# Optimization experiments

Hardware: AMD Instinct MI355X
Metric: run time of the kernel (lower is better)

## Reference

```python
import jax, jax.numpy as jnp
import numpy as np

MAX_DEPTH = 12  # 2^12-1 = 4095 internal nodes, 4096 leaves
NUM_INPUT = 1024
NUM_OUTPUT = 1024
BATCH = 4096


def setup_inputs() -> dict:
    key = jax.random.key(0)
    k1, k2, k3 = jax.random.split(key, 3)
    n_internal = (1 << MAX_DEPTH) - 1
    n_leaves = 1 << MAX_DEPTH
    x = jax.random.normal(k1, (BATCH, NUM_INPUT), dtype=jnp.float32)
    # per-node weights ~ N(0, 0.1) as in nn.Parameter(torch.empty(num_input).normal_(0, 0.1))
    W = jax.random.normal(k2, (n_internal, NUM_INPUT), dtype=jnp.float32) * 0.1
    b = jnp.zeros((n_internal,), dtype=jnp.float32)
    # leaf prob_dist initialized to ones in the original
    leaf = jnp.ones((n_leaves, NUM_OUTPUT), dtype=jnp.float32)
    # use random leaves so the blend is non-trivial for correctness checking
    leaf = leaf + jax.random.normal(k3, (n_leaves, NUM_OUTPUT), dtype=jnp.float32)
    return {"x": x, "W": W, "b": b, "leaf": leaf}


def reference(x, W, b, leaf):
    # W rows are internal nodes in level order: [root | level1 (2) | level2 (4) | ...]
    # Gate value at each node: sigmoid(x . w + b); output blends right with weight g,
    # left with weight (1-g), recursively -> leaf mixture weights are products of
    # gate / (1-gate) along each root-to-leaf path.
    B = x.shape[0]
    g = jax.nn.sigmoid(jnp.einsum('bi,ni->bn', x, W) + b)  # [B, n_internal]
    probs = jnp.ones((B, 1), dtype=x.dtype)
    idx = 0
    for d in range(MAX_DEPTH):  # structural loop over tree levels (fixed, small)
        n = 1 << d
        gl = g[:, idx:idx + n]  # gates at level d, [B, n]
        idx += n
        # children interleaved: [L0, R0, L1, R1, ...]; left weight (1-g), right g
        probs = jnp.stack([probs * (1.0 - gl), probs * gl], axis=-1).reshape(B, 2 * n)
    # output = sum over leaves of path_prob * leaf_dist
    out = jnp.einsum('bl,lo->bo', probs, leaf)  # [B, num_output]
    return out
```

## Files before the change

kernel.cpp:

```cpp
#include <hip/hip_runtime.h>
#include <hip/hip_bf16.h>
#include <hip/hip_fp16.h>

typedef _Float16 half8 __attribute__((ext_vector_type(8)));
typedef _Float16 half4 __attribute__((ext_vector_type(4)));
typedef float floatx4 __attribute__((ext_vector_type(4)));

#define BATCH   4096
#define NIN     1024
#define NODES   4095
#define NPAD    4096
#define NOUT    1024
#define NLEAF   4096
#define SPLITK  4

__device__ __forceinline__ void gload_lds16(const void* g, void* l) {
    __builtin_amdgcn_global_load_lds(
        (const __attribute__((address_space(1))) void*)g,
        (__attribute__((address_space(3))) void*)l, 16, 0, 0);
}

__global__ void k_prep(const float* __restrict__ x, const float* __restrict__ W,
                       const float* __restrict__ leaf,
                       _Float16* __restrict__ xh, _Float16* __restrict__ Wh,
                       _Float16* __restrict__ leafT) {
    __shared__ _Float16 t[32][33];
    const int b = blockIdx.x;
    if (b < 4096) {
        int i = (b * 256 + threadIdx.x) * 4;
        float4 v = *(const float4*)(x + i);
        half4 h;
        h.x = (_Float16)v.x; h.y = (_Float16)v.y;
        h.z = (_Float16)v.z; h.w = (_Float16)v.w;
        *(half4*)(xh + i) = h;
    } else if (b < 8192) {
        int i = ((b - 4096) * 256 + threadIdx.x) * 4;
        float4 v;
        if (i < NODES * NIN) v = *(const float4*)(W + i);
        else                 v = make_float4(0.f, 0.f, 0.f, 0.f);
        half4 h;
        h.x = (_Float16)v.x; h.y = (_Float16)v.y;
        h.z = (_Float16)v.z; h.w = (_Float16)v.w;
        *(half4*)(Wh + i) = h;
    } else {
        int tb = b - 8192;
        int l0 = (tb & 127) * 32, o0 = (tb >> 7) * 32;
        int tx = threadIdx.x & 31, ty = threadIdx.x >> 5;
#pragma unroll
        for (int i = 0; i < 4; i++) {
            int l = l0 + ty + i * 8;
            t[ty + i * 8][tx] = (_Float16)leaf[(size_t)l * NOUT + o0 + tx];
        }
        __syncthreads();
#pragma unroll
        for (int i = 0; i < 4; i++) {
            int o = o0 + ty + i * 8;
            leafT[(size_t)o * NLEAF + l0 + tx] = t[tx][ty + i * 8];
        }
    }
}

template <int EPILOGUE>
__launch_bounds__(1024, 4)
__global__ void gemm256(const _Float16* __restrict__ A,
                        const _Float16* __restrict__ Bm,
                        const float* __restrict__ bias,
                        void* __restrict__ C,
                        int M, int N, int K, int ldc, int Klen) {
    __shared__ __align__(16) _Float16 As[2 * 16384];
    __shared__ __align__(16) _Float16 Bs[2 * 16384];
    const int tid  = threadIdx.x;
    const int lane = tid & 63;
    const int wid  = tid >> 6;
    const int wm   = wid >> 2;
    const int wn   = wid & 3;
    const int m0 = blockIdx.y * 256;
    const int n0 = blockIdx.x * 256;
    const int k0 = blockIdx.z * Klen;
    (void)N;

    floatx4 acc[4][4] = {};

    const int hh = tid >> 9;
    const int rr = (tid >> 2) & 127;
    const int cc = (tid & 3) ^ ((tid >> 3) & 3);
    const _Float16* Abase = A  + (size_t)(m0 + hh * 128 + rr) * K + k0 + cc * 8;
    const _Float16* Bbase = Bm + (size_t)(n0 + hh * 128 + rr) * K + k0 + cc * 8;
    const int dsl = hh * 8192 + (tid & 511) * 8;

    auto stage = [&](int bufx, int T) {
        const int d = bufx * 16384 + dsl;
        gload_lds16(Abase + T * 64,      &As[d]);
        gload_lds16(Abase + T * 64 + 32, &As[d + 4096]);
        gload_lds16(Bbase + T * 64,      &Bs[d]);
        gload_lds16(Bbase + T * 64 + 32, &Bs[d + 4096]);
    };

    const int l15 = lane & 15;
    const int l4  = lane >> 4;
    const int pos = (l4 ^ ((l15 >> 1) & 3)) * 8;
    const int aoff = ((wm & 1) * 64 + l15) * 32 + pos + (wm >> 1) * 8192;
    const int boff = ((wn & 1) * 64 + l15) * 32 + pos + (wn >> 1) * 8192;

    auto compute = [&](int bufx) {
#pragma unroll
        for (int s = 0; s < 2; s++) {
            const _Float16* Ab = &As[bufx * 16384 + s * 4096 + aoff];
            const _Float16* Bb = &Bs[bufx * 16384 + s * 4096 + boff];
            half8 af[4], bf[4];
#pragma unroll
            for (int fi = 0; fi < 4; fi++)
                af[fi] = *(const half8*)(Ab + fi * 512);
#pragma unroll
            for (int fj = 0; fj < 4; fj++)
                bf[fj] = *(const half8*)(Bb + fj * 512);
#pragma unroll
            for (int fi = 0; fi < 4; fi++)
#pragma unroll
                for (int fj = 0; fj < 4; fj++)
                    acc[fi][fj] = __builtin_amdgcn_mfma_f32_16x16x32_f16(
                        af[fi], bf[fj], acc[fi][fj], 0, 0, 0);
        }
    };

    const int NTt = Klen >> 6;

    stage(0, 0);
    __syncthreads();
    for (int T = 0; T < NTt; T += 2) {
        if (T + 1 < NTt) stage(1, T + 1);
        compute(0);
        __syncthreads();
        if (T + 2 < NTt) stage(0, T + 2);
        if (T + 1 < NTt) compute(1);
        __syncthreads();
    }

    _Float16* Cp = (_Float16*)C + (EPILOGUE == 2 ? (size_t)blockIdx.z * M * ldc : 0);
#pragma unroll
    for (int fi = 0; fi < 4; fi++)
#pragma unroll
        for (int fj = 0; fj < 4; fj++) {
            const int col = n0 + wn * 64 + fj * 16 + l15;
            float bb = 0.f;
            if (EPILOGUE == 1) bb = (col < NODES) ? bias[col] : 0.f;
#pragma unroll
            for (int rj = 0; rj < 4; rj++) {
                const int row = m0 + wm * 64 + fi * 16 + l4 * 4 + rj;
                float v = acc[fi][fj][rj];
                if (EPILOGUE == 1) {
                    float z = v + bb;
                    Cp[(size_t)row * ldc + col] = (_Float16)(1.f / (1.f + __expf(-z)));
                } else {
                    Cp[(size_t)row * ldc + col] = (_Float16)v;
                }
            }
        }
}

__global__ void k_reduce4(const _Float16* __restrict__ part, float* __restrict__ out) {
    const size_t S = (size_t)BATCH * NOUT;
    size_t i = ((size_t)blockIdx.x * 256 + threadIdx.x) * 8;
    half8 a = *(const half8*)(part + i);
    half8 b = *(const half8*)(part + S + i);
    half8 c = *(const half8*)(part + 2 * S + i);
    half8 d = *(const half8*)(part + 3 * S + i);
    float4 lo, hi;
    lo.x = (float)a[0] + (float)b[0] + (float)c[0] + (float)d[0];
    lo.y = (float)a[1] + (float)b[1] + (float)c[1] + (float)d[1];
    lo.z = (float)a[2] + (float)b[2] + (float)c[2] + (float)d[2];
    lo.w = (float)a[3] + (float)b[3] + (float)c[3] + (float)d[3];
    hi.x = (float)a[4] + (float)b[4] + (float)c[4] + (float)d[4];
    hi.y = (float)a[5] + (float)b[5] + (float)c[5] + (float)d[5];
    hi.z = (float)a[6] + (float)b[6] + (float)c[6] + (float)d[6];
    hi.w = (float)a[7] + (float)b[7] + (float)c[7] + (float)d[7];
    *(float4*)(out + i) = lo;
    *(float4*)(out + i + 4) = hi;
}

__global__ void k_probs(const _Float16* __restrict__ g,
                        _Float16* __restrict__ probs) {
    __shared__ float gs[NPAD];
    const int b = blockIdx.x;
    const _Float16* grow = g + (size_t)b * NPAD;
#pragma unroll
    for (int it = 0; it < 2; it++) {
        int i = threadIdx.x + it * 256;
        half8 v = *(const half8*)(grow + i * 8);
#pragma unroll
        for (int j = 0; j < 8; j++) gs[i * 8 + j] = (float)v[j];
    }
    __syncthreads();
    const int t = threadIdx.x;
    float p = 1.f;
#pragma unroll
    for (int d = 0; d < 8; d++) {
        int node = (1 << d) - 1 + (t >> (8 - d));
        float gg = gs[node];
        int bit = (t >> (7 - d)) & 1;
        p *= bit ? gg : (1.f - gg);
    }
    float p9[2], p10[4], p11[8], p12[16];
    {
        float gg = gs[255 + t];
        p9[0] = p * (1.f - gg); p9[1] = p * gg;
    }
#pragma unroll
    for (int i = 0; i < 2; i++) {
        float gg = gs[511 + 2 * t + i];
        p10[2 * i] = p9[i] * (1.f - gg); p10[2 * i + 1] = p9[i] * gg;
    }
#pragma unroll
    for (int i = 0; i < 4; i++) {
        float gg = gs[1023 + 4 * t + i];
        p11[2 * i] = p10[i] * (1.f - gg); p11[2 * i + 1] = p10[i] * gg;
    }
#pragma unroll
    for (int i = 0; i < 8; i++) {
        float gg = gs[2047 + 8 * t + i];
        p12[2 * i] = p11[i] * (1.f - gg); p12[2 * i + 1] = p11[i] * gg;
    }
    half8 o0, o1;
#pragma unroll
    for (int j = 0; j < 8; j++) { o0[j] = (_Float16)p12[j]; o1[j] = (_Float16)p12[8 + j]; }
    _Float16* pr = probs + (size_t)b * NLEAF + t * 16;
    *(half8*)(pr) = o0;
    *(half8*)(pr + 8) = o1;
}

extern "C" void kernel_launch(void* const* d_in, const int* in_sizes, int n_in,
                              void* d_out, int out_size, void* d_ws, size_t ws_size,
                              hipStream_t stream) {
    (void)in_sizes; (void)n_in; (void)out_size; (void)ws_size;
    const float* x    = (const float*)d_in[0];
    const float* W    = (const float*)d_in[1];
    const float* bias = (const float*)d_in[2];
    const float* leaf = (const float*)d_in[3];
    float* out = (float*)d_out;

    _Float16* base  = (_Float16*)d_ws;
    _Float16* leafT = base;
    _Float16* probs = base + (size_t)4 * 1024 * 1024;
    _Float16* xh    = base + (size_t)20 * 1024 * 1024;
    _Float16* Wh    = base + (size_t)24 * 1024 * 1024;
    _Float16* g     = base + (size_t)28 * 1024 * 1024;
    _Float16* part  = xh;

    k_prep<<<12288, 256, 0, stream>>>(x, W, leaf, xh, Wh, leafT);

    gemm256<1><<<dim3(NPAD / 256, BATCH / 256, 1), 1024, 0, stream>>>(
        xh, Wh, bias, (void*)g, BATCH, NPAD, NIN, NPAD, NIN);

    k_probs<<<BATCH, 256, 0, stream>>>(g, probs);

    gemm256<2><<<dim3(NOUT / 256, BATCH / 256, SPLITK), 1024, 0, stream>>>(
        probs, leafT, nullptr, (void*)part, BATCH, NOUT, NLEAF, NOUT, NLEAF / SPLITK);

    k_reduce4<<<(BATCH * NOUT) / (256 * 8), 256, 0, stream>>>(part, out);
}
```

Baseline: 109.9 us.

## Switch GEMM to triple-buffered 32-wide K tiles with one raw barrier per step

```diff
diff --git a/kernel.cpp b/kernel.cpp
--- a/kernel.cpp
+++ b/kernel.cpp
@@ -19,6 +19,8 @@
         (const __attribute__((address_space(1))) void*)g,
         (__attribute__((address_space(3))) void*)l, 16, 0, 0);
 }
+
+#define RBAR() asm volatile("s_barrier" ::: "memory")
 
 __global__ void k_prep(const float* __restrict__ x, const float* __restrict__ W,
                        const float* __restrict__ leaf,
@@ -67,8 +69,8 @@
                         const float* __restrict__ bias,
                         void* __restrict__ C,
                         int M, int N, int K, int ldc, int Klen) {
-    __shared__ __align__(16) _Float16 As[2 * 16384];
-    __shared__ __align__(16) _Float16 Bs[2 * 16384];
+    __shared__ __align__(16) _Float16 As[3 * 8192];
+    __shared__ __align__(16) _Float16 Bs[3 * 8192];
     const int tid  = threadIdx.x;
     const int lane = tid & 63;
     const int wid  = tid >> 6;
@@ -81,60 +83,63 @@
 
     floatx4 acc[4][4] = {};
 
-    const int hh = tid >> 9;
-    const int rr = (tid >> 2) & 127;
+    const int rr = tid >> 2;
     const int cc = (tid & 3) ^ ((tid >> 3) & 3);
-    const _Float16* Abase = A  + (size_t)(m0 + hh * 128 + rr) * K + k0 + cc * 8;
-    const _Float16* Bbase = Bm + (size_t)(n0 + hh * 128 + rr) * K + k0 + cc * 8;
-    const int dsl = hh * 8192 + (tid & 511) * 8;
+    const _Float16* Abase = A  + (size_t)(m0 + rr) * K + k0 + cc * 8;
+    const _Float16* Bbase = Bm + (size_t)(n0 + rr) * K + k0 + cc * 8;
+    const int dsl = tid * 8;
 
     auto stage = [&](int bufx, int T) {
-        const int d = bufx * 16384 + dsl;
-        gload_lds16(Abase + T * 64,      &As[d]);
-        gload_lds16(Abase + T * 64 + 32, &As[d + 4096]);
-        gload_lds16(Bbase + T * 64,      &Bs[d]);
-        gload_lds16(Bbase + T * 64 + 32, &Bs[d + 4096]);
+        gload_lds16(Abase + T * 32, &As[bufx * 8192 + dsl]);
+        gload_lds16(Bbase + T * 32, &Bs[bufx * 8192 + dsl]);
     };
 
     const int l15 = lane & 15;
     const int l4  = lane >> 4;
     const int pos = (l4 ^ ((l15 >> 1) & 3)) * 8;
-    const int aoff = ((wm & 1) * 64 + l15) * 32 + pos + (wm >> 1) * 8192;
-    const int boff = ((wn & 1) * 64 + l15) * 32 + pos + (wn >> 1) * 8192;
+    const int aoff = (wm * 64 + l15) * 32 + pos;
+    const int boff = (wn * 64 + l15) * 32 + pos;
 
     auto compute = [&](int bufx) {
-#pragma unroll
-        for (int s = 0; s < 2; s++) {
-            const _Float16* Ab = &As[bufx * 16384 + s * 4096 + aoff];
-            const _Float16* Bb = &Bs[bufx * 16384 + s * 4096 + boff];
-            half8 af[4], bf[4];
-#pragma unroll
-            for (int fi = 0; fi < 4; fi++)
-                af[fi] = *(const half8*)(Ab + fi * 512);
+        const _Float16* Ab = &As[bufx * 8192 + aoff];
+        const _Float16* Bb = &Bs[bufx * 8192 + boff];
+        half8 af[4], bf[4];
+#pragma unroll
+        for (int fi = 0; fi < 4; fi++)
+            af[fi] = *(const half8*)(Ab + fi * 512);
+#pragma unroll
+        for (int fj = 0; fj < 4; fj++)
+            bf[fj] = *(const half8*)(Bb + fj * 512);
+        __builtin_amdgcn_s_setprio(1);
+#pragma unroll
+        for (int fi = 0; fi < 4; fi++)
 #pragma unroll
             for (int fj = 0; fj < 4; fj++)
-                bf[fj] = *(const half8*)(Bb + fj * 512);
-#pragma unroll
-            for (int fi = 0; fi < 4; fi++)
-#pragma unroll
-                for (int fj = 0; fj < 4; fj++)
-                    acc[fi][fj] = __builtin_amdgcn_mfma_f32_16x16x32_f16(
-                        af[fi], bf[fj], acc[fi][fj], 0, 0, 0);
-        }
+                acc[fi][fj] = __builtin_amdgcn_mfma_f32_16x16x32_f16(
+                    af[fi], bf[fj], acc[fi][fj], 0, 0, 0);
+        __builtin_amdgcn_s_setprio(0);
     };
 
-    const int NTt = Klen >> 6;
-
-    stage(0, 0);
-    __syncthreads();
-    for (int T = 0; T < NTt; T += 2) {
-        if (T + 1 < NTt) stage(1, T + 1);
-        compute(0);
-        __syncthreads();
-        if (T + 2 < NTt) stage(0, T + 2);
-        if (T + 1 < NTt) compute(1);
-        __syncthreads();
-    }
+    const int NT = Klen >> 5;
+
+#define PHASE(B, T)                                                             \
+    {                                                                           \
+        if ((T) + 2 < NT) stage((B + 2) % 3, (T) + 2);                          \
+        compute(B);                                                             \
+        if ((T) + 2 < NT)      asm volatile("s_waitcnt vmcnt(2)" ::: "memory"); \
+        else if ((T) + 1 < NT) asm volatile("s_waitcnt vmcnt(0)" ::: "memory"); \
+        if ((T) + 1 < NT) RBAR();                                               \
+    }
+
+    stage(0, 0); stage(1, 1);
+    asm volatile("s_waitcnt vmcnt(2)" ::: "memory");
+    RBAR();
+
+    for (int T = 0; T < 30; T += 3) {
+        PHASE(0, T); PHASE(1, T + 1); PHASE(2, T + 2);
+    }
+    PHASE(0, 30); PHASE(1, 31);
+#undef PHASE
 
     _Float16* Cp = (_Float16*)C + (EPILOGUE == 2 ? (size_t)blockIdx.z * M * ldc : 0);
 #pragma unroll
```

Measured after the change: 118.1 us. 1.07x slower.

## Split-K the gate GEMM with BK32 tiles and separate bias-sigmoid reduction

Applied to the files above, without the earlier changes.

```diff
diff --git a/kernel.cpp b/kernel.cpp
--- a/kernel.cpp
+++ b/kernel.cpp
@@ -60,13 +60,92 @@
     }
 }
 
-template <int EPILOGUE>
+__launch_bounds__(1024, 8)
+__global__ void gemm_bk32(const _Float16* __restrict__ A,
+                          const _Float16* __restrict__ Bm,
+                          _Float16* __restrict__ C,
+                          int M, int N, int K, int ldc, int Klen) {
+    __shared__ __align__(16) _Float16 As[2 * 8192];
+    __shared__ __align__(16) _Float16 Bs[2 * 8192];
+    const int tid  = threadIdx.x;
+    const int lane = tid & 63;
+    const int wid  = tid >> 6;
+    const int wm   = wid >> 2;
+    const int wn   = wid & 3;
+    const int m0 = blockIdx.y * 256;
+    const int n0 = blockIdx.x * 256;
+    const int k0 = blockIdx.z * Klen;
+    (void)N;
+
+    floatx4 acc[4][4] = {};
+
+    const int rr = tid >> 2;
+    const int cc = (tid & 3) ^ ((tid >> 3) & 3);
+    const _Float16* Abase = A  + (size_t)(m0 + rr) * K + k0 + cc * 8;
+    const _Float16* Bbase = Bm + (size_t)(n0 + rr) * K + k0 + cc * 8;
+    const int dsl = tid * 8;
+
+    auto stage = [&](int bufx, int T) {
+        gload_lds16(Abase + T * 32, &As[bufx * 8192 + dsl]);
+        gload_lds16(Bbase + T * 32, &Bs[bufx * 8192 + dsl]);
+    };
+
+    const int l15 = lane & 15;
+    const int l4  = lane >> 4;
+    const int pos = (l4 ^ ((l15 >> 1) & 3)) * 8;
+    const int aoff = (wm * 64 + l15) * 32 + pos;
+    const int boff = (wn * 64 + l15) * 32 + pos;
+
+    auto compute = [&](int bufx) {
+        const _Float16* Ab = &As[bufx * 8192 + aoff];
+        const _Float16* Bb = &Bs[bufx * 8192 + boff];
+        half8 af[4], bf[4];
+#pragma unroll
+        for (int fi = 0; fi < 4; fi++)
+            af[fi] = *(const half8*)(Ab + fi * 512);
+#pragma unroll
+        for (int fj = 0; fj < 4; fj++)
+            bf[fj] = *(const half8*)(Bb + fj * 512);
+#pragma unroll
+        for (int fi = 0; fi < 4; fi++)
+#pragma unroll
+            for (int fj = 0; fj < 4; fj++)
+                acc[fi][fj] = __builtin_amdgcn_mfma_f32_16x16x32_f16(
+                    af[fi], bf[fj], acc[fi][fj], 0, 0, 0);
+    };
+
+    const int NT = Klen >> 5;
+
+    stage(0, 0);
+    __syncthreads();
+    for (int T = 0; T < NT; T += 2) {
+        if (T + 1 < NT) stage(1, T + 1);
+        compute(0);
+        __syncthreads();
+        if (T + 2 < NT) stage(0, T + 2);
+        if (T + 1 < NT) compute(1);
+        __syncthreads();
+    }
+
+    _Float16* Cp = C + (size_t)blockIdx.z * M * ldc;
+#pragma unroll
+    for (int fi = 0; fi < 4; fi++)
+#pragma unroll
+        for (int fj = 0; fj < 4; fj++) {
+            const int col = n0 + wn * 64 + fj * 16 + l15;
+#pragma unroll
+            for (int rj = 0; rj < 4; rj++) {
+                const int row = m0 + wm * 64 + fi * 16 + l4 * 4 + rj;
+                Cp[(size_t)row * ldc + col] = (_Float16)acc[fi][fj][rj];
+            }
+        }
+}
+
 __launch_bounds__(1024, 4)
-__global__ void gemm256(const _Float16* __restrict__ A,
-                        const _Float16* __restrict__ Bm,
-                        const float* __restrict__ bias,
-                        void* __restrict__ C,
-                        int M, int N, int K, int ldc, int Klen) {
+__global__ void gemm_bk64(const _Float16* __restrict__ A,
+                          const _Float16* __restrict__ Bm,
+                          _Float16* __restrict__ C,
+                          int M, int N, int K, int ldc, int Klen) {
     __shared__ __align__(16) _Float16 As[2 * 16384];
     __shared__ __align__(16) _Float16 Bs[2 * 16384];
     const int tid  = threadIdx.x;
@@ -136,26 +215,45 @@
         __syncthreads();
     }
 
-    _Float16* Cp = (_Float16*)C + (EPILOGUE == 2 ? (size_t)blockIdx.z * M * ldc : 0);
+    _Float16* Cp = C + (size_t)blockIdx.z * M * ldc;
 #pragma unroll
     for (int fi = 0; fi < 4; fi++)
 #pragma unroll
         for (int fj = 0; fj < 4; fj++) {
             const int col = n0 + wn * 64 + fj * 16 + l15;
-            float bb = 0.f;
-            if (EPILOGUE == 1) bb = (col < NODES) ? bias[col] : 0.f;
 #pragma unroll
             for (int rj = 0; rj < 4; rj++) {
                 const int row = m0 + wm * 64 + fi * 16 + l4 * 4 + rj;
-                float v = acc[fi][fj][rj];
-                if (EPILOGUE == 1) {
-                    float z = v + bb;
-                    Cp[(size_t)row * ldc + col] = (_Float16)(1.f / (1.f + __expf(-z)));
-                } else {
-                    Cp[(size_t)row * ldc + col] = (_Float16)v;
-                }
+                Cp[(size_t)row * ldc + col] = (_Float16)acc[fi][fj][rj];
             }
         }
+}
+
+__global__ void k_reduce2_sig(const _Float16* __restrict__ pg,
+                              const float* __restrict__ bias,
+                              _Float16* __restrict__ g) {
+    const size_t S = (size_t)BATCH * NPAD;
+    size_t i = ((size_t)blockIdx.x * 256 + threadIdx.x) * 8;
+    half8 a = *(const half8*)(pg + i);
+    half8 b = *(const half8*)(pg + S + i);
+    const int col = (int)(i & (NPAD - 1));
+    float bb[8];
+    if (col + 8 <= NODES) {
+        float4 b0 = *(const float4*)(bias + col);
+        float4 b1 = *(const float4*)(bias + col + 4);
+        bb[0] = b0.x; bb[1] = b0.y; bb[2] = b0.z; bb[3] = b0.w;
+        bb[4] = b1.x; bb[5] = b1.y; bb[6] = b1.z; bb[7] = b1.w;
+    } else {
+#pragma unroll
+        for (int j = 0; j < 8; j++) bb[j] = (col + j < NODES) ? bias[col + j] : 0.f;
+    }
+    half8 o;
+#pragma unroll
+    for (int j = 0; j < 8; j++) {
+        float z = (float)a[j] + (float)b[j] + bb[j];
+        o[j] = (_Float16)(1.f / (1.f + __expf(-z)));
+    }
+    *(half8*)(g + i) = o;
 }
 
 __global__ void k_reduce4(const _Float16* __restrict__ part, float* __restrict__ out) {
@@ -239,22 +337,25 @@
     float* out = (float*)d_out;
 
     _Float16* base  = (_Float16*)d_ws;
-    _Float16* leafT = base;
-    _Float16* probs = base + (size_t)4 * 1024 * 1024;
-    _Float16* xh    = base + (size_t)20 * 1024 * 1024;
-    _Float16* Wh    = base + (size_t)24 * 1024 * 1024;
-    _Float16* g     = base + (size_t)28 * 1024 * 1024;
-    _Float16* part  = xh;
+    _Float16* xh    = base;
+    _Float16* Wh    = base + (size_t)4  * 1024 * 1024;
+    _Float16* leafT = base + (size_t)8  * 1024 * 1024;
+    _Float16* pg    = base + (size_t)12 * 1024 * 1024;
+    _Float16* g     = pg;
+    _Float16* probs = base + (size_t)28 * 1024 * 1024;
+    _Float16* part  = base + (size_t)12 * 1024 * 1024;
 
     k_prep<<<12288, 256, 0, stream>>>(x, W, leaf, xh, Wh, leafT);
 
-    gemm256<1><<<dim3(NPAD / 256, BATCH / 256, 1), 1024, 0, stream>>>(
-        xh, Wh, bias, (void*)g, BATCH, NPAD, NIN, NPAD, NIN);
+    gemm_bk32<<<dim3(NPAD / 256, BATCH / 256, 2), 1024, 0, stream>>>(
+        xh, Wh, pg, BATCH, NPAD, NIN, NPAD, NIN / 2);
+
+    k_reduce2_sig<<<(BATCH * NPAD) / (256 * 8), 256, 0, stream>>>(pg, bias, g);
 
     k_probs<<<BATCH, 256, 0, stream>>>(g, probs);
 
-    gemm256<2><<<dim3(NOUT / 256, BATCH / 256, SPLITK), 1024, 0, stream>>>(
-        probs, leafT, nullptr, (void*)part, BATCH, NOUT, NLEAF, NOUT, NLEAF / SPLITK);
+    gemm_bk64<<<dim3(NOUT / 256, BATCH / 256, SPLITK), 1024, 0, stream>>>(
+        probs, leafT, part, BATCH, NOUT, NLEAF, NOUT, NLEAF / SPLITK);
 
     k_reduce4<<<(BATCH * NOUT) / (256 * 8), 256, 0, stream>>>(part, out);
 }
```

After: 425.6 us. +287.2%, slower.
